# Kernel optimization log

Hardware: AMD Instinct MI355X
Metric: run time of the kernel (lower is better)

The kernel has to match this reference:

```python
import jax, jax.numpy as jnp
import numpy as np

B, NH, M, XD = 8192, 128, 4096, 1024
ALPHA_1, SIGMA_1 = 100.0, 0.02
MAX_ITER = 30  # FastBarrierProjectionNoUpper(max_iter=30)


def cayley(W):
    """Cayley orthogonalization of a (possibly rectangular) matrix (out, in)."""
    cout, cin = W.shape
    if cout < cin:
        return cayley(W.T).T
    U, V = W[:cin], W[cin:]                 # U: (cin,cin), V: (cout-cin,cin)
    I = jnp.eye(cin, dtype=W.dtype)
    A = U - U.T + V.T @ V                   # skew + Gram
    iIpA = jnp.linalg.inv(I + A)
    return jnp.concatenate([iIpA @ (I - A), -2.0 * V @ iIpA], axis=0)


def cayley_linear(x, W, b, alpha):
    Q = cayley(alpha * W / jnp.linalg.norm(W))
    return x @ Q.T + b


def project_no_upper(lower, f_tilde):
    """Projection of f_tilde onto {f : sum(f)=0, f >= lower} per row.
    f*(lam) = max(f_tilde - lam, lower); Newton on g(lam)=sum f*(lam)=0,
    iterated a fixed MAX_ITER times (matches the 30-iter barrier solver)."""
    lam0 = jnp.mean(f_tilde, axis=-1, keepdims=True)

    def step(lam, _):
        f = jnp.maximum(f_tilde - lam, lower)
        g = jnp.sum(f, axis=-1, keepdims=True)
        active = jnp.sum((f_tilde - lam > lower).astype(f.dtype), axis=-1, keepdims=True)
        dg = -jnp.maximum(active, 1.0)      # g'(lam), safeguarded
        return lam - g / dg, None

    lam, _ = jax.lax.scan(step, lam0, None, length=MAX_ITER)
    return jnp.maximum(f_tilde - lam, lower)


def setup_inputs() -> dict:
    key = jax.random.key(0)
    ks = jax.random.split(key, 8)
    h = jax.random.uniform(ks[0], (B, NH), dtype=jnp.float32)
    h = h / jnp.sum(h, axis=-1, keepdims=True)      # state lives on the simplex
    x = jax.random.normal(ks[1], (B, XD), dtype=jnp.float32)

    def mk_w(k, shape):
        return jax.random.normal(k, shape, dtype=jnp.float32) * 0.05

    W_hm = mk_w(ks[2], (M, NH))
    W_mm = mk_w(ks[3], (M, M))
    W_mh = mk_w(ks[4], (NH, M))
    W_ux = mk_w(ks[5], (M, XD))
    b_hm = jnp.zeros((M,), jnp.float32)
    b_mm = jnp.zeros((M,), jnp.float32)
    b_mh = jnp.zeros((NH,), jnp.float32)
    b_ux = jnp.zeros((M,), jnp.float32)
    # CayleyLinear alpha initialized to ||W||_F (so alpha*W/||W|| == W at init)
    a_hm = jnp.linalg.norm(W_hm)
    a_mm = jnp.linalg.norm(W_mm)
    a_mh = jnp.linalg.norm(W_mh)
    a_ux = jnp.linalg.norm(W_ux)
    return {"h": h, "x": x,
            "W_hm": W_hm, "b_hm": b_hm, "a_hm": a_hm,
            "W_mm": W_mm, "b_mm": b_mm, "a_mm": a_mm,
            "W_mh": W_mh, "b_mh": b_mh, "a_mh": a_mh,
            "W_ux": W_ux, "b_ux": b_ux, "a_ux": a_ux}


def reference(h, x, W_hm, b_hm, a_hm, W_mm, b_mm, a_mm,
              W_mh, b_mh, a_mh, W_ux, b_ux, a_ux):
    # _h_dot_raw (dropout identity in eval mode)
    z = cayley_linear(h, W_hm, b_hm, a_hm) + cayley_linear(x, W_ux, b_ux, a_ux)
    z = jax.nn.relu(z)
    z = jax.nn.relu(cayley_linear(z, W_mm, b_mm, a_mm))
    f_tilde = cayley_linear(z, W_mh, b_mh, a_mh)   # [B, NH]
    # barrier lower bound keeping h >= 0 forward-invariant
    lower = -ALPHA_1 * (jnp.exp(SIGMA_1 * h) - 1.0)
    return project_no_upper(lower, f_tilde)
```

## Files before the change

### kernel.cpp

```cpp
#include <hip/hip_runtime.h>
#include <math.h>

#define ALPHA_1 100.0f
#define SIGMA_1 0.02f

typedef unsigned short bf16_t;
typedef short  bf16x8  __attribute__((ext_vector_type(8)));
typedef float  floatx4 __attribute__((ext_vector_type(4)));

typedef __attribute__((address_space(1))) void glb_void;
typedef __attribute__((address_space(3))) void lds_void;

__device__ __forceinline__ float bf2f(bf16_t u){ return __uint_as_float(((unsigned)u)<<16); }
__device__ __forceinline__ bf16_t f2bf(float f){
  unsigned u = __float_as_uint(f);
  u += 0x7FFFu + ((u>>16)&1u);
  return (bf16_t)(u>>16);
}

__device__ __forceinline__ void split4(float4 v, ushort4& h, ushort4& l){
  h.x=f2bf(v.x); h.y=f2bf(v.y); h.z=f2bf(v.z); h.w=f2bf(v.w);
  l.x=f2bf(v.x-bf2f(h.x)); l.y=f2bf(v.y-bf2f(h.y));
  l.z=f2bf(v.z-bf2f(h.z)); l.w=f2bf(v.w-bf2f(h.w));
}

__device__ __forceinline__ float4 load4f(const float* p){ return *(const float4*)p; }
__device__ __forceinline__ float loadS(const float* p){ return *p; }
__device__ __forceinline__ float loadS(const bf16_t* p){ return bf2f(*p); }
__device__ __forceinline__ void storeS(float* p, float v){ *p = v; }
__device__ __forceinline__ void storeS(bf16_t* p, float v){ *p = f2bf(v); }

__device__ __forceinline__ void async_copy16(void* lds, const void* g){
  __builtin_amdgcn_global_load_lds((glb_void*)g, (lds_void*)lds, 16, 0, 0);
}

template<typename TC, int RELU>
__global__ __launch_bounds__(256) void mfma_nt_kernel(
    int Mm, int Nn, int Kk,
    const bf16_t* __restrict__ A, int lda,
    const bf16_t* __restrict__ B, int ldb,
    TC* __restrict__ C, int ldc,
    const float* __restrict__ bias)
{
  __shared__ bf16_t As[128*64];
  __shared__ bf16_t Bs[128*64];
  const int tid  = threadIdx.x;
  const int lane = tid & 63, wv = tid >> 6;
  const int m0 = (int)(blockIdx.y << 7), n0 = (int)(blockIdx.x << 7);
  const int wm = (wv >> 1) << 6, wn = (wv & 1) << 6;
  const int rbase = wv << 5;

  floatx4 acc[4][4] = {};

  for (int kk = 0; kk < Kk; kk += 64){
    __syncthreads();
#pragma unroll
    for (int q=0;q<4;q++){
      int row = rbase + (q<<3) + (lane>>3);
      int cg  = (lane&7) ^ (row&7);
      async_copy16(&As[(size_t)(rbase+(q<<3))<<6],
                   A + (size_t)(m0+row)*lda + kk + (cg<<3));
      async_copy16(&Bs[(size_t)(rbase+(q<<3))<<6],
                   B + (size_t)(n0+row)*ldb + kk + (cg<<3));
    }
    __syncthreads();
#pragma unroll
    for (int ks=0; ks<2; ks++){
      bf16x8 af[4], bf[4];
      int quad = lane>>4, mr = lane&15;
      int c = quad + (ks<<2);
#pragma unroll
      for (int i=0;i<4;i++){
        int rowa = wm + i*16 + mr;
        af[i] = *(const bf16x8*)&As[(rowa<<6) + ((c ^ (rowa&7))<<3)];
        int rowb = wn + i*16 + mr;
        bf[i] = *(const bf16x8*)&Bs[(rowb<<6) + ((c ^ (rowb&7))<<3)];
      }
#pragma unroll
      for (int i=0;i<4;i++)
#pragma unroll
        for (int j=0;j<4;j++)
          acc[i][j] = __builtin_amdgcn_mfma_f32_16x16x32_bf16(af[i], bf[j], acc[i][j], 0,0,0);
    }
  }
#pragma unroll
  for (int i=0;i<4;i++){
#pragma unroll
    for (int j=0;j<4;j++){
      int rbase2 = m0 + wm + i*16 + (lane>>4)*4;
      int col    = n0 + wn + j*16 + (lane&15);
      float bv = bias ? bias[col] : 0.0f;
#pragma unroll
      for (int r=0;r<4;r++){
        float v = acc[i][j][r] + bv;
        if (RELU) v = fmaxf(v, 0.0f);
        storeS(&C[(size_t)(rbase2+r)*ldc + col], v);
      }
    }
  }
}

template<typename TC>
__global__ __launch_bounds__(256) void fgemm_nt_kernel(
    int Mm, int Nn, int Kk,
    const float* __restrict__ A, int lda,
    const float* __restrict__ Bt, int ldb,
    TC* __restrict__ C, int ldc,
    float alpha, const float* __restrict__ alpha_ptr, float beta, int skipk)
{
  __shared__ bf16_t Ah[128*64], Al[128*64], Bh[128*64], Bl[128*64];
  const int tid = threadIdx.x;
  const int lane = tid & 63, wv = tid >> 6;
  int by = blockIdx.y; if (by >= skipk) by++;
  const int m0 = by << 7, n0 = blockIdx.x << 7;
  const int wm = (wv >> 1) << 6, wn = (wv & 1) << 6;
  floatx4 acc[4][4] = {};

  for (int kk = 0; kk < Kk; kk += 64){
    float4 va[8], vb[8];
#pragma unroll
    for (int i=0;i<8;i++){
      int idx = (tid<<3) + i;
      int row = idx >> 4;
      int cg  = idx & 15;
      va[i] = load4f(A  + (size_t)(m0+row)*lda + kk + (cg<<2));
      vb[i] = load4f(Bt + (size_t)(n0+row)*ldb + kk + (cg<<2));
    }
    __syncthreads();
#pragma unroll
    for (int i=0;i<8;i++){
      int idx = (tid<<3) + i;
      int row = idx >> 4, cg = idx & 15;
      int off = (row<<6) + (((cg>>1) ^ (row&7))<<3) + ((cg&1)<<2);
      ushort4 hv, lv; split4(va[i], hv, lv);
      *(ushort4*)&Ah[off] = hv; *(ushort4*)&Al[off] = lv;
      ushort4 hw, lw; split4(vb[i], hw, lw);
      *(ushort4*)&Bh[off] = hw; *(ushort4*)&Bl[off] = lw;
    }
    __syncthreads();
#pragma unroll
    for (int ks=0; ks<2; ks++){
      int quad = lane>>4, mr = lane&15;
      int c = quad + (ks<<2);
      bf16x8 ah[4], al[4], bh[4], bl[4];
#pragma unroll
      for (int i=0;i<4;i++){
        int rowa = wm + i*16 + mr; int sa = (rowa<<6) + ((c ^ (rowa&7))<<3);
        ah[i] = *(const bf16x8*)&Ah[sa]; al[i] = *(const bf16x8*)&Al[sa];
        int rowb = wn + i*16 + mr; int sb = (rowb<<6) + ((c ^ (rowb&7))<<3);
        bh[i] = *(const bf16x8*)&Bh[sb]; bl[i] = *(const bf16x8*)&Bl[sb];
      }
#pragma unroll
      for (int i=0;i<4;i++)
#pragma unroll
        for (int j=0;j<4;j++){
          acc[i][j] = __builtin_amdgcn_mfma_f32_16x16x32_bf16(ah[i], bl[j], acc[i][j], 0,0,0);
          acc[i][j] = __builtin_amdgcn_mfma_f32_16x16x32_bf16(al[i], bh[j], acc[i][j], 0,0,0);
          acc[i][j] = __builtin_amdgcn_mfma_f32_16x16x32_bf16(ah[i], bh[j], acc[i][j], 0,0,0);
        }
    }
    __syncthreads();
  }
  float am = alpha;
  if (alpha_ptr) am *= *alpha_ptr;
#pragma unroll
  for (int i=0;i<4;i++){
#pragma unroll
    for (int j=0;j<4;j++){
      int rb = m0 + wm + i*16 + (lane>>4)*4;
      int col = n0 + wn + j*16 + (lane&15);
#pragma unroll
      for (int r=0;r<4;r++){
        size_t off = (size_t)(rb+r)*ldc + col;
        float v = am * acc[i][j][r];
        if (beta != 0.0f) v = fmaf(beta, loadS(&C[off]), v);
        storeS(&C[off], v);
      }
    }
  }
}

__global__ __launch_bounds__(1024) void invert128_kernel(
    const float* __restrict__ src, int ld,
    float* __restrict__ dst, float* __restrict__ dstT)
{
  __shared__ float brow[2][8*36];
  const int t = threadIdx.x;
  const int r = t>>3, sub = t&7;
  const int lane = t & 63;
  const int cb = (sub&3)<<5;
  const bool isA = sub < 4;
  float own[32];
  if (isA){
#pragma unroll
    for (int i=0;i<32;i++) own[i] = src[(size_t)r*ld + cb + i];
  } else {
#pragma unroll
    for (int i=0;i<32;i++) own[i] = (cb+i == r) ? 1.0f : 0.0f;
  }
  for (int pb=0; pb<4; pb++){
#pragma unroll
    for (int pi=0; pi<32; pi++){
      const int p = (pb<<5) + pi;
      float f = __shfl(own[pi], (lane & 56) | pb);
      float* bw = brow[p & 1];
      if (r == p){
        float ip = 1.0f / f;
#pragma unroll
        for (int i=0;i<32;i++) own[i] *= ip;
#pragma unroll
        for (int i=0;i<8;i++){
          float4 v;
          v.x = own[(i<<2)+0]; v.y = own[(i<<2)+1];
          v.z = own[(i<<2)+2]; v.w = own[(i<<2)+3];
          *(float4*)&bw[sub*36 + (i<<2)] = v;
        }
      }
      __syncthreads();
      if (r != p){
#pragma unroll
        for (int i=0;i<8;i++){
          float4 b = *(const float4*)&bw[sub*36 + (i<<2)];
          own[(i<<2)+0] = fmaf(-f, b.x, own[(i<<2)+0]);
          own[(i<<2)+1] = fmaf(-f, b.y, own[(i<<2)+1]);
          own[(i<<2)+2] = fmaf(-f, b.z, own[(i<<2)+2]);
          own[(i<<2)+3] = fmaf(-f, b.w, own[(i<<2)+3]);
        }
      }
    }
  }
  if (!isA){
#pragma unroll
    for (int i=0;i<32;i++){
      dst [(size_t)r*128 + cb + i] = own[i];
      dstT[(size_t)(cb+i)*128 + r] = own[i];
    }
  }
}

__global__ __launch_bounds__(1024) void gj_prepL_kernel(
    const float* __restrict__ Mc, int n, int k,
    bf16_t* __restrict__ Gh, bf16_t* __restrict__ Gl,
    bf16_t* __restrict__ Th, bf16_t* __restrict__ Tl)
{
  __shared__ float brow[2][8*36];
  __shared__ float Pl[128*132];
  __shared__ float Ast[128*132];
  const int t = threadIdx.x;
  const int ib = blockIdx.x;
  const int r = t>>3, sub = t&7;
  const int lane = t & 63;
  const int cb = (sub&3)<<5;
  const bool isA = sub < 4;
  const float* D = Mc + ((size_t)(k<<7))*n + (k<<7);
  float own[32];
  if (isA){
#pragma unroll
    for (int q=0;q<32;q++) own[q] = D[(size_t)r*n + cb + q];
  } else {
#pragma unroll
    for (int q=0;q<32;q++) own[q] = (cb+q == r) ? 1.0f : 0.0f;
  }
  for (int pb=0; pb<4; pb++){
#pragma unroll
    for (int pi=0; pi<32; pi++){
      const int p = (pb<<5) + pi;
      float f = __shfl(own[pi], (lane & 56) | pb);
      float* bw = brow[p & 1];
      if (r == p){
        float ip = 1.0f / f;
#pragma unroll
        for (int q=0;q<32;q++) own[q] *= ip;
#pragma unroll
        for (int q=0;q<8;q++){
          float4 v;
          v.x=own[(q<<2)+0]; v.y=own[(q<<2)+1]; v.z=own[(q<<2)+2]; v.w=own[(q<<2)+3];
          *(float4*)&bw[sub*36 + (q<<2)] = v;
        }
      }
      __syncthreads();
      if (r != p){
#pragma unroll
        for (int q=0;q<8;q++){
          float4 b = *(const float4*)&bw[sub*36 + (q<<2)];
          own[(q<<2)+0] = fmaf(-f, b.x, own[(q<<2)+0]);
          own[(q<<2)+1] = fmaf(-f, b.y, own[(q<<2)+1]);
          own[(q<<2)+2] = fmaf(-f, b.z, own[(q<<2)+2]);
          own[(q<<2)+3] = fmaf(-f, b.w, own[(q<<2)+3]);
        }
      }
    }
  }
  if (!isA){
#pragma unroll
    for (int q=0;q<8;q++){
      float4 v;
      v.x=own[(q<<2)+0]; v.y=own[(q<<2)+1]; v.z=own[(q<<2)+2]; v.w=own[(q<<2)+3];
      *(float4*)&Pl[r*132 + cb + (q<<2)] = v;
      if (ib == k){
        ushort4 hv, lv; split4(v, hv, lv);
        *(ushort4*)&Gh[((size_t)k<<14) + (r<<7) + cb + (q<<2)] = hv;
        *(ushort4*)&Gl[((size_t)k<<14) + (r<<7) + cb + (q<<2)] = lv;
      }
    }
  }
  __syncthreads();
  if (ib == k) return;

  const float* Ski = Mc + ((size_t)(k<<7))*n + (ib<<7);
#pragma unroll
  for (int q=0;q<4;q++){
    int f4 = (t<<2) + q;
    int rr = f4>>5, c4 = (f4&31)<<2;
    *(float4*)&Ast[rr*132 + c4] = *(const float4*)&Ski[(size_t)rr*n + c4];
  }
  __syncthreads();
#pragma unroll
  for (int q=0;q<4;q++){
    int f4 = (t<<2) + q;
    int cc = f4>>5, r4 = (f4&31)<<2;
    float4 v;
    v.x = Ast[(r4+0)*132 + cc]; v.y = Ast[(r4+1)*132 + cc];
    v.z = Ast[(r4+2)*132 + cc]; v.w = Ast[(r4+3)*132 + cc];
    ushort4 hv, lv; split4(v, hv, lv);
    *(ushort4*)&Th[((size_t)ib<<14) + (cc<<7) + r4] = hv;
    *(ushort4*)&Tl[((size_t)ib<<14) + (cc<<7) + r4] = lv;
  }
  __syncthreads();

  const float* Sik = Mc + ((size_t)(ib<<7))*n + (k<<7);
#pragma unroll
  for (int q=0;q<4;q++){
    int f4 = (t<<2) + q;
    int rr = f4>>5, c4 = (f4&31)<<2;
    *(float4*)&Ast[rr*132 + c4] = *(const float4*)&Sik[(size_t)rr*n + c4];
  }
  __syncthreads();

  const int tx = t&31, ty = t>>5;
  const int r0 = ty<<2, c0 = tx<<2;
  float acc[4][4] = {};
  for (int kq=0; kq<128; kq++){
    float4 b = *(const float4*)&Pl[kq*132 + c0];
    float a0 = Ast[(r0+0)*132 + kq];
    float a1 = Ast[(r0+1)*132 + kq];
    float a2 = Ast[(r0+2)*132 + kq];
    float a3 = Ast[(r0+3)*132 + kq];
    acc[0][0]=fmaf(a0,b.x,acc[0][0]); acc[0][1]=fmaf(a0,b.y,acc[0][1]);
    acc[0][2]=fmaf(a0,b.z,acc[0][2]); acc[0][3]=fmaf(a0,b.w,acc[0][3]);
    acc[1][0]=fmaf(a1,b.x,acc[1][0]); acc[1][1]=fmaf(a1,b.y,acc[1][1]);
    acc[1][2]=fmaf(a1,b.z,acc[1][2]); acc[1][3]=fmaf(a1,b.w,acc[1][3]);
    acc[2][0]=fmaf(a2,b.x,acc[2][0]); acc[2][1]=fmaf(a2,b.y,acc[2][1]);
    acc[2][2]=fmaf(a2,b.z,acc[2][2]); acc[2][3]=fmaf(a2,b.w,acc[2][3]);
    acc[3][0]=fmaf(a3,b.x,acc[3][0]); acc[3][1]=fmaf(a3,b.y,acc[3][1]);
    acc[3][2]=fmaf(a3,b.z,acc[3][2]); acc[3][3]=fmaf(a3,b.w,acc[3][3]);
  }
#pragma unroll
  for (int rr=0;rr<4;rr++){
    float4 v; v.x=-acc[rr][0]; v.y=-acc[rr][1]; v.z=-acc[rr][2]; v.w=-acc[rr][3];
    ushort4 hv, lv; split4(v, hv, lv);
    *(ushort4*)&Gh[((size_t)ib<<14) + ((size_t)(r0+rr)<<7) + c0] = hv;
    *(ushort4*)&Gl[((size_t)ib<<14) + ((size_t)(r0+rr)<<7) + c0] = lv;
  }
}

__global__ __launch_bounds__(256) void gj_update_kernel(
    const float* __restrict__ Min, float* __restrict__ Mout, int n, int k,
    const bf16_t* __restrict__ Gh, const bf16_t* __restrict__ Gl,
    const bf16_t* __restrict__ Th, const bf16_t* __restrict__ Tl)
{
  const int bx = blockIdx.x, by = blockIdx.y;
  const int tid = threadIdx.x;
  if (bx == k){
    const bf16_t* sh = Gh + ((size_t)by<<14);
    const bf16_t* sl = Gl + ((size_t)by<<14);
    float* dst = Mout + ((size_t)(by<<7))*n + ((size_t)k<<7);
    for (int q=tid; q<4096; q+=256){
      int r=q>>5, c4=(q&31)<<2;
      ushort4 hv=*(const ushort4*)&sh[(r<<7)+c4];
      ushort4 lv=*(const ushort4*)&sl[(r<<7)+c4];
      float4 v; v.x=bf2f(hv.x)+bf2f(lv.x); v.y=bf2f(hv.y)+bf2f(lv.y);
                v.z=bf2f(hv.z)+bf2f(lv.z); v.w=bf2f(hv.w)+bf2f(lv.w);
      *(float4*)&dst[(size_t)r*n + c4] = v;
    }
    return;
  }
  __shared__ bf16_t Ah[128*64], Al[128*64], Bh[128*64], Bl[128*64];
  const int lane = tid & 63, wv = tid >> 6;
  const int wm = (wv >> 1) << 6, wn = (wv & 1) << 6;
  const bf16_t* gh = Gh + ((size_t)by<<14);
  const bf16_t* gl = Gl + ((size_t)by<<14);
  const bf16_t* th = Th + ((size_t)bx<<14);
  const bf16_t* tl = Tl + ((size_t)bx<<14);
  floatx4 acc[4][4] = {};

#pragma unroll
  for (int kk = 0; kk < 128; kk += 64){
    __syncthreads();
#pragma unroll
    for (int i=0;i<8;i++){
      int idx = (tid<<3) + i;
      int row = idx >> 4, cg = idx & 15;
      int off = (row<<6) + (((cg>>1) ^ (row&7))<<3) + ((cg&1)<<2);
      *(ushort4*)&Ah[off] = *(const ushort4*)&gh[(row<<7) + kk + (cg<<2)];
      *(ushort4*)&Al[off] = *(const ushort4*)&gl[(row<<7) + kk + (cg<<2)];
      *(ushort4*)&Bh[off] = *(const ushort4*)&th[(row<<7) + kk + (cg<<2)];
      *(ushort4*)&Bl[off] = *(const ushort4*)&tl[(row<<7) + kk + (cg<<2)];
    }
    __syncthreads();
#pragma unroll
    for (int ks=0; ks<2; ks++){
      int quad = lane>>4, mr = lane&15;
      int c = quad + (ks<<2);
      bf16x8 ah[4], al[4], bh[4], bl[4];
#pragma unroll
      for (int i=0;i<4;i++){
        int rowa = wm + i*16 + mr; int sa = (rowa<<6) + ((c ^ (rowa&7))<<3);
        ah[i] = *(const bf16x8*)&Ah[sa]; al[i] = *(const bf16x8*)&Al[sa];
        int rowb = wn + i*16 + mr; int sb = (rowb<<6) + ((c ^ (rowb&7))<<3);
        bh[i] = *(const bf16x8*)&Bh[sb]; bl[i] = *(const bf16x8*)&Bl[sb];
      }
#pragma unroll
      for (int i=0;i<4;i++)
#pragma unroll
        for (int j=0;j<4;j++){
          acc[i][j] = __builtin_amdgcn_mfma_f32_16x16x32_bf16(ah[i], bl[j], acc[i][j], 0,0,0);
          acc[i][j] = __builtin_amdgcn_mfma_f32_16x16x32_bf16(al[i], bh[j], acc[i][j], 0,0,0);
          acc[i][j] = __builtin_amdgcn_mfma_f32_16x16x32_bf16(ah[i], bh[j], acc[i][j], 0,0,0);
        }
    }
  }
  const int addin = (by != k);
#pragma unroll
  for (int i=0;i<4;i++)
#pragma unroll
    for (int j=0;j<4;j++){
      int rb = (by<<7) + wm + i*16 + ((lane>>4)<<2);
      int col = (bx<<7) + wn + j*16 + (lane&15);
#pragma unroll
      for (int r4=0;r4<4;r4++){
        size_t off = (size_t)(rb+r4)*n + col;
        float v = acc[i][j][r4];
        if (addin) v += Min[off];
        Mout[off] = v;
      }
    }
}

template<int TRANS>
__global__ __launch_bounds__(256) void gram_partial_kernel(
    const float* __restrict__ V, int ldv, int n, int Ks,
    float* __restrict__ Gp)
{
  __shared__ float Vi[16][132];
  __shared__ float Vj[16][132];
  const int cj = blockIdx.x, ci = blockIdx.y, z = blockIdx.z;
  const int tid = threadIdx.x;
  const int i0 = ci<<7, j0 = cj<<7;
  const int tx = tid&15, ty = tid>>4;
  float acc[8][8] = {};
  for (int k0 = z*Ks; k0 < (z+1)*Ks; k0 += 16){
    if (TRANS == 0){
      for (int q=tid; q<512; q+=256){
        int kr = q>>5, c4 = (q&31)<<2;
        *(float4*)&Vi[kr][c4] = *(const float4*)&V[(size_t)(k0+kr)*ldv + i0 + c4];
        *(float4*)&Vj[kr][c4] = *(const float4*)&V[(size_t)(k0+kr)*ldv + j0 + c4];
      }
    } else {
      for (int q=tid; q<512; q+=256){
        int c = q>>2, qq = (q&3)<<2;
        float4 a = *(const float4*)&V[(size_t)(i0+c)*ldv + k0 + qq];
        Vi[qq+0][c]=a.x; Vi[qq+1][c]=a.y; Vi[qq+2][c]=a.z; Vi[qq+3][c]=a.w;
        float4 b = *(const float4*)&V[(size_t)(j0+c)*ldv + k0 + qq];
        Vj[qq+0][c]=b.x; Vj[qq+1][c]=b.y; Vj[qq+2][c]=b.z; Vj[qq+3][c]=b.w;
      }
    }
    __syncthreads();
#pragma unroll
    for (int kr=0; kr<16; kr++){
      float a[8], b[8];
      *(float4*)&a[0] = *(const float4*)&Vi[kr][(ty<<3)];
      *(float4*)&a[4] = *(const float4*)&Vi[kr][(ty<<3)+4];
      *(float4*)&b[0] = *(const float4*)&Vj[kr][(tx<<3)];
      *(float4*)&b[4] = *(const float4*)&Vj[kr][(tx<<3)+4];
#pragma unroll
      for (int i=0;i<8;i++)
#pragma unroll
        for (int jj=0;jj<8;jj++) acc[i][jj] = fmaf(a[i], b[jj], acc[i][jj]);
    }
    __syncthreads();
  }
#pragma unroll
  for (int i=0;i<8;i++)
#pragma unroll
    for (int jj=0;jj<8;jj++)
      Gp[(size_t)z*n*n + (size_t)(i0+(ty<<3)+i)*n + j0+(tx<<3)+jj] = acc[i][jj];
}

__global__ void sumsq_kernel(const float* __restrict__ w, int n, float* __restrict__ acc){
  float s = 0.0f;
  for (int i = blockIdx.x*blockDim.x + threadIdx.x; i < n; i += gridDim.x*blockDim.x){
    float v = w[i]; s = fmaf(v, v, s);
  }
#pragma unroll
  for (int o=32;o;o>>=1) s += __shfl_xor(s, o);
  if ((threadIdx.x & 63) == 0) atomicAdd(acc, s);
}

__global__ void scales_kernel(float* scal, const float* a0, const float* a1,
                              const float* a2, const float* a3){
  if (threadIdx.x==0 && blockIdx.x==0){
    float s;
    s = a0[0]/sqrtf(scal[0]); scal[4]=s; scal[8]=s*s;
    s = a1[0]/sqrtf(scal[1]); scal[5]=s; scal[9]=s*s;
    s = a2[0]/sqrtf(scal[2]); scal[6]=s; scal[10]=s*s;
    s = a3[0]/sqrtf(scal[3]); scal[7]=s; scal[11]=s*s;
  }
}

__global__ void build_mm_kernel(const float* __restrict__ W, const float* __restrict__ scal,
                                float* __restrict__ Mo){
  int j = (blockIdx.x<<4) + (threadIdx.x&15);
  int i = (blockIdx.y<<4) + (threadIdx.x>>4);
  float s = scal[5];
  float a = s*(W[((size_t)i<<12)+j] - W[((size_t)j<<12)+i]);
  Mo[((size_t)i<<12)+j] = ((i==j)?1.0f:0.0f) + a;
}

__global__ void build_rect_kernel(const float* __restrict__ W, int ldw, int transw, int n,
      const float* __restrict__ Gp, int S,
      const float* __restrict__ scal, int sidx, int sidx2,
      float* __restrict__ Mo){
  int j = (blockIdx.x<<4)+(threadIdx.x&15);
  int i = (blockIdx.y<<4)+(threadIdx.x>>4);
  float s = scal[sidx], s2 = scal[sidx2];
  float wij = transw ? W[(size_t)j*ldw+i] : W[(size_t)i*ldw+j];
  float wji = transw ? W[(size_t)i*ldw+j] : W[(size_t)j*ldw+i];
  float g = 0.0f;
  for (int ss=0; ss<S; ss++) g += Gp[(size_t)ss*n*n + (size_t)i*n + j];
  Mo[(size_t)i*n + j] = ((i==j)?1.0f:0.0f) + s*(wij - wji) + s2*g;
}

template<typename TD>
__global__ void qtop_kernel(const float* __restrict__ X, int n,
                            TD* __restrict__ dst, int ldd){
  int j = blockIdx.x*blockDim.x + threadIdx.x;
  int i = blockIdx.y;
  if (j<n) storeS(&dst[(size_t)i*ldd+j],
                  2.0f*X[(size_t)i*n+j] - ((i==j)?1.0f:0.0f));
}

__global__ void transposeF_kernel(const float* __restrict__ src, int ls,
                                  float* __restrict__ dst, int ld){
  __shared__ float t[32][33];
  int c0 = blockIdx.x<<5, r0 = blockIdx.y<<5;
  int tx = threadIdx.x & 31, ty = threadIdx.x >> 5;
#pragma unroll
  for (int i=0;i<4;i++) t[ty+i*8][tx] = src[(size_t)(r0+ty+i*8)*ls + c0+tx];
  __syncthreads();
#pragma unroll
  for (int i=0;i<4;i++) dst[(size_t)(c0+ty+i*8)*ld + r0+tx] = t[tx][ty+i*8];
}

__global__ void pack_A_kernel(const float* __restrict__ h, const float* __restrict__ x,
                              bf16_t* __restrict__ Ap){
  int c = blockIdx.x*blockDim.x + threadIdx.x;
  int m = blockIdx.y;
  if (c >= 2176) return;
  float v;
  if (c < 128)       v = h[(size_t)m*128 + c];
  else if (c < 1152) v = x[(size_t)m*1024 + (c-128)];
  else {
    float xv = x[(size_t)m*1024 + (c-1152)];
    v = xv - bf2f(f2bf(xv));
  }
  Ap[(size_t)m*2176 + c] = f2bf(v);
}

__global__ void dup_kernel(bf16_t* __restrict__ Bp){
  int c = blockIdx.x*blockDim.x + threadIdx.x;
  int r = blockIdx.y;
  Bp[(size_t)r*2176 + 1152 + c] = Bp[(size_t)r*2176 + 128 + c];
}

__global__ void addvec_kernel(const float* __restrict__ a, const float* __restrict__ b,
                              float* __restrict__ c, int n){
  int i = blockIdx.x*blockDim.x + threadIdx.x;
  if (i<n) c[i] = a[i] + b[i];
}

__global__ __launch_bounds__(256) void project_kernel(
    const float* __restrict__ ft, const float* __restrict__ h, float* __restrict__ out){
  int row  = (blockIdx.x<<2) + (threadIdx.x>>6);
  int lane = threadIdx.x & 63;
  const float* fr = ft + ((size_t)row<<7);
  const float* hr = h  + ((size_t)row<<7);
  float f0 = fr[lane], f1 = fr[lane+64];
  float l0 = -ALPHA_1*(expf(SIGMA_1*hr[lane])   - 1.0f);
  float l1 = -ALPHA_1*(expf(SIGMA_1*hr[lane+64])- 1.0f);
  float s = f0 + f1;
#pragma unroll
  for (int o=32;o;o>>=1) s += __shfl_xor(s, o);
  float lam = s * (1.0f/128.0f);
  for (int it=0; it<30; it++){
    float a0 = f0 - lam, a1 = f1 - lam;
    float g = fmaxf(a0,l0) + fmaxf(a1,l1);
    float c = (a0>l0 ? 1.0f:0.0f) + (a1>l1 ? 1.0f:0.0f);
#pragma unroll
    for (int o=32;o;o>>=1){ g += __shfl_xor(g,o); c += __shfl_xor(c,o); }
    lam += g / fmaxf(c, 1.0f);
  }
  out[((size_t)row<<7)+lane]    = fmaxf(f0-lam, l0);
  out[((size_t)row<<7)+lane+64] = fmaxf(f1-lam, l1);
}

template<typename TC, int RELU>
static inline void mfma_nt(hipStream_t st, int Mm, int Nn, int Kk,
    const bf16_t* A, int lda, const bf16_t* B, int ldb, TC* C, int ldc,
    const float* bias){
  dim3 grid(Nn>>7, Mm>>7);
  mfma_nt_kernel<TC,RELU><<<grid, 256, 0, st>>>(Mm,Nn,Kk,A,lda,B,ldb,C,ldc,bias);
}

template<typename TC>
static inline void fgemm(hipStream_t st, int Mm, int Nn, int Kk,
    const float* A, int lda, const float* Bt, int ldb, TC* C, int ldc,
    float alpha, const float* aptr, float beta){
  dim3 grid(Nn>>7, Mm>>7);
  fgemm_nt_kernel<TC><<<grid, 256, 0, st>>>(Mm,Nn,Kk,A,lda,Bt,ldb,C,ldc,
                                            alpha,aptr,beta, 1<<30);
}

static void gj_inverse2(hipStream_t st, float* M, float* Mtmp, int n,
                        bf16_t* Gh, bf16_t* Gl, bf16_t* Th, bf16_t* Tl){
  int nb = n >> 7;
  float* cur = M; float* nxt = Mtmp;
  for (int k=0;k<nb;k++){
    gj_prepL_kernel<<<nb, 1024, 0, st>>>(cur, n, k, Gh, Gl, Th, Tl);
    dim3 grid(nb, nb);
    gj_update_kernel<<<grid, 256, 0, st>>>(cur, nxt, n, k, Gh, Gl, Th, Tl);
    float* t = cur; cur = nxt; nxt = t;
  }
}

extern "C" void kernel_launch(void* const* d_in, const int* in_sizes, int n_in,
                              void* d_out, int out_size, void* d_ws, size_t ws_size,
                              hipStream_t stream){
  (void)in_sizes; (void)n_in; (void)out_size; (void)ws_size;
  const float* h    = (const float*)d_in[0];
  const float* x    = (const float*)d_in[1];
  const float* Whm  = (const float*)d_in[2];
  const float* bhm  = (const float*)d_in[3];
  const float* ahm  = (const float*)d_in[4];
  const float* Wmm  = (const float*)d_in[5];
  const float* bmm  = (const float*)d_in[6];
  const float* amm  = (const float*)d_in[7];
  const float* Wmh  = (const float*)d_in[8];
  const float* bmh  = (const float*)d_in[9];
  const float* amh  = (const float*)d_in[10];
  const float* Wux  = (const float*)d_in[11];
  const float* bux  = (const float*)d_in[12];
  const float* auxs = (const float*)d_in[13];
  float* out = (float*)d_out;

  char* wp = (char*)d_ws;
  auto alloc = [&](size_t bytes)->void*{
    void* p = (void*)wp; wp += (bytes + 255) & ~(size_t)255; return p; };
  float*  scal   = (float*)alloc(4096);
  float*  Mhm    = (float*)alloc((size_t)128*128*4);
  float*  Mmh    = (float*)alloc((size_t)128*128*4);
  float*  P128   = (float*)alloc((size_t)128*128*4);
  float*  PT128  = (float*)alloc((size_t)128*128*4);
  bf16_t* GhB    = (bf16_t*)alloc((size_t)32*16384*2);
  bf16_t* GlB    = (bf16_t*)alloc((size_t)32*16384*2);
  bf16_t* ThB    = (bf16_t*)alloc((size_t)32*16384*2);
  bf16_t* TlB    = (bf16_t*)alloc((size_t)32*16384*2);
  bf16_t* Qmh_b  = (bf16_t*)alloc((size_t)128*4096*2);
  float*  bsum   = (float*)alloc((size_t)4096*4);
  bf16_t* Bp     = (bf16_t*)alloc((size_t)4096*2176*2);
  float*  R1     = (float*)alloc((size_t)4096*4096*4);
  float*  R2     = (float*)alloc((size_t)4096*4096*4);
  bf16_t* Qmmb   = (bf16_t*)alloc((size_t)4096*4096*2);
  float*  gram23 = R1;
  float*  WmhTv  = R1 + (size_t)1024*1024;
  float*  Mmm  = R1;
  bf16_t* Ap   = (bf16_t*)R1;
  bf16_t* z2   = (bf16_t*)R1;
  float*  Mux  = R2 + (size_t)1024*1024;
  float*  XuxT = R2 + (size_t)5*1024*1024;
  float*  Gp1  = R2 + (size_t)6*1024*1024;
  bf16_t* z    = (bf16_t*)R2;
  float*  ftl  = R2;

  hipMemsetAsync(scal, 0, 16*sizeof(float), stream);
  sumsq_kernel<<<512,256,0,stream>>>(Whm, 4096*128,  scal+0);
  sumsq_kernel<<<512,256,0,stream>>>(Wmm, 4096*4096, scal+1);
  sumsq_kernel<<<512,256,0,stream>>>(Wmh, 128*4096,  scal+2);
  sumsq_kernel<<<512,256,0,stream>>>(Wux, 4096*1024, scal+3);
  scales_kernel<<<1,1,0,stream>>>(scal, ahm, amm, amh, auxs);

  gram_partial_kernel<0><<<dim3(8,8,4),256,0,stream>>>(
      Wux + (size_t)1024*1024, 1024, 1024, 768, Gp1);
  build_rect_kernel<<<dim3(64,64),256,0,stream>>>(Wux,1024,0,1024, Gp1,4, scal,7,11, Mux);
  gj_inverse2(stream, Mux, R1, 1024, GhB, GlB, ThB, TlB);
  transposeF_kernel<<<dim3(32,32),256,0,stream>>>(Mux, 1024, XuxT, 1024);
  qtop_kernel<bf16_t><<<dim3(4,1024),256,0,stream>>>(Mux, 1024, Bp+128, 2176);
  fgemm<bf16_t>(stream, 3072,1024,1024, Wux+(size_t)1024*1024,1024, XuxT,1024,
                Bp+(size_t)1024*2176+128, 2176, -2.0f,&scal[7], 0.0f);

  gram_partial_kernel<0><<<dim3(1,1,31),256,0,stream>>>(
      Whm + (size_t)128*128, 128, 128, 128, gram23);
  build_rect_kernel<<<dim3(8,8),256,0,stream>>>(Whm,128,0,128, gram23,31, scal,4,8, Mhm);
  invert128_kernel<<<1,1024,0,stream>>>(Mhm,128,P128,PT128);
  qtop_kernel<bf16_t><<<dim3(1,128),256,0,stream>>>(P128, 128, Bp, 2176);
  fgemm<bf16_t>(stream, 3968,128,128, Whm+128*128,128, PT128,128,
                Bp+(size_t)128*2176, 2176, -2.0f,&scal[4], 0.0f);

  gram_partial_kernel<1><<<dim3(1,1,31),256,0,stream>>>(
      Wmh + 128, 4096, 128, 128, gram23);
  build_rect_kernel<<<dim3(8,8),256,0,stream>>>(Wmh,4096,1,128, gram23,31, scal,6,10, Mmh);
  invert128_kernel<<<1,1024,0,stream>>>(Mmh,128,P128,PT128);
  qtop_kernel<bf16_t><<<dim3(1,128),256,0,stream>>>(PT128, 128, Qmh_b, 4096);
  transposeF_kernel<<<dim3(124,4),256,0,stream>>>(Wmh+128, 4096, WmhTv, 128);
  fgemm<bf16_t>(stream, 128,3968,128, PT128,128, WmhTv,128,
                Qmh_b+128, 4096, -2.0f,&scal[6], 0.0f);

  build_mm_kernel<<<dim3(256,256),256,0,stream>>>(Wmm, scal, Mmm);
  gj_inverse2(stream, Mmm, R2, 4096, GhB, GlB, ThB, TlB);
  qtop_kernel<bf16_t><<<dim3(16,4096),256,0,stream>>>(Mmm, 4096, Qmmb, 4096);

  pack_A_kernel<<<dim3(9,8192),256,0,stream>>>(h, x, Ap);
  dup_kernel<<<dim3(4,4096),256,0,stream>>>(Bp);
  addvec_kernel<<<16,256,0,stream>>>(bhm, bux, bsum, 4096);

  mfma_nt<bf16_t,1>(stream, 8192,4096,2176, Ap,2176, Bp,2176, z,4096, bsum);
  mfma_nt<bf16_t,1>(stream, 8192,4096,4096, z,4096, Qmmb,4096, z2,4096, bmm);
  mfma_nt<float,0>(stream, 8192, 128,4096, z2,4096, Qmh_b,4096, ftl,128, bmh);

  project_kernel<<<2048,256,0,stream>>>(ftl, h, out);
}
```

Measured before the change: 6.347 ms.

## Pipeline block Gauss-Jordan: fuse next-panel prep with trailing update

Restructures the blocked Gauss-Jordan inverse so that each step first updates the next pivot block-column and row (stepA). A second kernel then runs the next panel's prep concurrently with the rest of the trailing update (stepB), using double-buffered G/T panel buffers. This removes the serial single-row-of-blocks prep launch between update launches, where only nb blocks kept the GPU busy. Update tiles now use 1024-thread blocks with a 2x2 MFMA tile per wave instead of 256 threads with 4x4. That changes occupancy and register use, and the heavy prep blocks may become stragglers inside stepB.

Result: faster. 5.696 ms (-10.3%).

```diff
diff --git a/kernel.cpp b/kernel.cpp
--- a/kernel.cpp
+++ b/kernel.cpp
@@ -238,16 +238,16 @@
   }
 }
 
-__global__ __launch_bounds__(1024) void gj_prepL_kernel(
-    const float* __restrict__ Mc, int n, int k,
+
+__device__ void prep1024(
+    const float* __restrict__ Mc, int n, int k, int ib,
     bf16_t* __restrict__ Gh, bf16_t* __restrict__ Gl,
-    bf16_t* __restrict__ Th, bf16_t* __restrict__ Tl)
-{
-  __shared__ float brow[2][8*36];
-  __shared__ float Pl[128*132];
-  __shared__ float Ast[128*132];
-  const int t = threadIdx.x;
-  const int ib = blockIdx.x;
+    bf16_t* __restrict__ Th, bf16_t* __restrict__ Tl,
+    char* smraw, int t)
+{
+  float* browB = (float*)smraw;
+  float* Pl    = (float*)(smraw + 2304);
+  float* Ast   = (float*)(smraw + 69888);
   const int r = t>>3, sub = t&7;
   const int lane = t & 63;
   const int cb = (sub&3)<<5;
@@ -266,7 +266,7 @@
     for (int pi=0; pi<32; pi++){
       const int p = (pb<<5) + pi;
       float f = __shfl(own[pi], (lane & 56) | pb);
-      float* bw = brow[p & 1];
+      float* bw = browB + (p & 1)*288;
       if (r == p){
         float ip = 1.0f / f;
 #pragma unroll
@@ -364,18 +364,18 @@
   }
 }
 
-__global__ __launch_bounds__(256) void gj_update_kernel(
+__device__ void update_tile1024(
     const float* __restrict__ Min, float* __restrict__ Mout, int n, int k,
+    int by, int bx,
     const bf16_t* __restrict__ Gh, const bf16_t* __restrict__ Gl,
-    const bf16_t* __restrict__ Th, const bf16_t* __restrict__ Tl)
-{
-  const int bx = blockIdx.x, by = blockIdx.y;
-  const int tid = threadIdx.x;
+    const bf16_t* __restrict__ Th, const bf16_t* __restrict__ Tl,
+    char* sm, int tid)
+{
   if (bx == k){
     const bf16_t* sh = Gh + ((size_t)by<<14);
     const bf16_t* sl = Gl + ((size_t)by<<14);
     float* dst = Mout + ((size_t)(by<<7))*n + ((size_t)k<<7);
-    for (int q=tid; q<4096; q+=256){
+    for (int q=tid; q<4096; q+=1024){
       int r=q>>5, c4=(q&31)<<2;
       ushort4 hv=*(const ushort4*)&sh[(r<<7)+c4];
       ushort4 lv=*(const ushort4*)&sl[(r<<7)+c4];
@@ -385,21 +385,22 @@
     }
     return;
   }
-  __shared__ bf16_t Ah[128*64], Al[128*64], Bh[128*64], Bl[128*64];
+  bf16_t* Ah=(bf16_t*)sm;           bf16_t* Al=(bf16_t*)(sm+16384);
+  bf16_t* Bh=(bf16_t*)(sm+32768);   bf16_t* Bl=(bf16_t*)(sm+49152);
   const int lane = tid & 63, wv = tid >> 6;
-  const int wm = (wv >> 1) << 6, wn = (wv & 1) << 6;
+  const int wm = (wv >> 2) << 5, wn = (wv & 3) << 5;
   const bf16_t* gh = Gh + ((size_t)by<<14);
   const bf16_t* gl = Gl + ((size_t)by<<14);
   const bf16_t* th = Th + ((size_t)bx<<14);
   const bf16_t* tl = Tl + ((size_t)bx<<14);
-  floatx4 acc[4][4] = {};
+  floatx4 acc[2][2] = {};
 
 #pragma unroll
   for (int kk = 0; kk < 128; kk += 64){
     __syncthreads();
 #pragma unroll
-    for (int i=0;i<8;i++){
-      int idx = (tid<<3) + i;
+    for (int s=0;s<2;s++){
+      int idx = tid + (s<<10);
       int row = idx >> 4, cg = idx & 15;
       int off = (row<<6) + (((cg>>1) ^ (row&7))<<3) + ((cg&1)<<2);
       *(ushort4*)&Ah[off] = *(const ushort4*)&gh[(row<<7) + kk + (cg<<2)];
@@ -412,18 +413,18 @@
     for (int ks=0; ks<2; ks++){
       int quad = lane>>4, mr = lane&15;
       int c = quad + (ks<<2);
-      bf16x8 ah[4], al[4], bh[4], bl[4];
-#pragma unroll
-      for (int i=0;i<4;i++){
+      bf16x8 ah[2], al[2], bh[2], bl[2];
+#pragma unroll
+      for (int i=0;i<2;i++){
         int rowa = wm + i*16 + mr; int sa = (rowa<<6) + ((c ^ (rowa&7))<<3);
         ah[i] = *(const bf16x8*)&Ah[sa]; al[i] = *(const bf16x8*)&Al[sa];
         int rowb = wn + i*16 + mr; int sb = (rowb<<6) + ((c ^ (rowb&7))<<3);
         bh[i] = *(const bf16x8*)&Bh[sb]; bl[i] = *(const bf16x8*)&Bl[sb];
       }
 #pragma unroll
-      for (int i=0;i<4;i++)
-#pragma unroll
-        for (int j=0;j<4;j++){
+      for (int i=0;i<2;i++)
+#pragma unroll
+        for (int j=0;j<2;j++){
           acc[i][j] = __builtin_amdgcn_mfma_f32_16x16x32_bf16(ah[i], bl[j], acc[i][j], 0,0,0);
           acc[i][j] = __builtin_amdgcn_mfma_f32_16x16x32_bf16(al[i], bh[j], acc[i][j], 0,0,0);
           acc[i][j] = __builtin_amdgcn_mfma_f32_16x16x32_bf16(ah[i], bh[j], acc[i][j], 0,0,0);
@@ -432,9 +433,9 @@
   }
   const int addin = (by != k);
 #pragma unroll
-  for (int i=0;i<4;i++)
-#pragma unroll
-    for (int j=0;j<4;j++){
+  for (int i=0;i<2;i++)
+#pragma unroll
+    for (int j=0;j<2;j++){
       int rb = (by<<7) + wm + i*16 + ((lane>>4)<<2);
       int col = (bx<<7) + wn + j*16 + (lane&15);
 #pragma unroll
@@ -445,6 +446,59 @@
         Mout[off] = v;
       }
     }
+}
+
+__global__ __launch_bounds__(1024) void gj_prep0_kernel(
+    const float* __restrict__ M, int n,
+    bf16_t* Gh, bf16_t* Gl, bf16_t* Th, bf16_t* Tl)
+{
+  __shared__ char sm[137472] __attribute__((aligned(16)));
+  prep1024(M, n, 0, blockIdx.x, Gh, Gl, Th, Tl, sm, threadIdx.x);
+}
+
+__global__ __launch_bounds__(1024) void gj_stepA_kernel(
+    const float* __restrict__ Min, float* __restrict__ Mout, int n, int k,
+    const bf16_t* __restrict__ Gh, const bf16_t* __restrict__ Gl,
+    const bf16_t* __restrict__ Th, const bf16_t* __restrict__ Tl)
+{
+  __shared__ char sm[65536] __attribute__((aligned(16)));
+  const int nb = n >> 7;
+  const int bid = blockIdx.x;
+  int by, bx;
+  if (bid < nb){ by = bid; bx = k+1; }
+  else { by = k+1; bx = bid-nb; if (bx >= k+1) bx++; }
+  update_tile1024(Min, Mout, n, k, by, bx, Gh, Gl, Th, Tl, sm, threadIdx.x);
+}
+
+__global__ __launch_bounds__(1024) void gj_stepB_kernel(
+    const float* __restrict__ Min, float* __restrict__ Mout, int n, int k,
+    const bf16_t* __restrict__ Gh, const bf16_t* __restrict__ Gl,
+    const bf16_t* __restrict__ Th, const bf16_t* __restrict__ Tl,
+    bf16_t* Gnh, bf16_t* Gnl, bf16_t* Tnh, bf16_t* Tnl)
+{
+  __shared__ char sm[137472] __attribute__((aligned(16)));
+  const int nb = n >> 7;
+  const int bid = blockIdx.x, tid = threadIdx.x;
+  if (bid < nb){
+    prep1024(Mout, n, k+1, bid, Gnh, Gnl, Tnh, Tnl, sm, tid);
+  } else {
+    int q = bid - nb;
+    int by = q/(nb-1), bx = q - by*(nb-1);
+    if (by >= k+1) by++;
+    if (bx >= k+1) bx++;
+    update_tile1024(Min, Mout, n, k, by, bx, Gh, Gl, Th, Tl, sm, tid);
+  }
+}
+
+__global__ __launch_bounds__(1024) void gj_stepL_kernel(
+    const float* __restrict__ Min, float* __restrict__ Mout, int n, int k,
+    const bf16_t* __restrict__ Gh, const bf16_t* __restrict__ Gl,
+    const bf16_t* __restrict__ Th, const bf16_t* __restrict__ Tl)
+{
+  __shared__ char sm[65536] __attribute__((aligned(16)));
+  const int nb = n >> 7;
+  int by = blockIdx.x / nb, bx = blockIdx.x - by*nb;
+  update_tile1024(Min, Mout, n, k, by, bx, Gh, Gl, Th, Tl, sm, threadIdx.x);
 }
 
 template<int TRANS>
@@ -631,15 +685,25 @@
                                             alpha,aptr,beta, 1<<30);
 }
 
-static void gj_inverse2(hipStream_t st, float* M, float* Mtmp, int n,
-                        bf16_t* Gh, bf16_t* Gl, bf16_t* Th, bf16_t* Tl){
-  int nb = n >> 7;
-  float* cur = M; float* nxt = Mtmp;
-  for (int k=0;k<nb;k++){
-    gj_prepL_kernel<<<nb, 1024, 0, st>>>(cur, n, k, Gh, Gl, Th, Tl);
-    dim3 grid(nb, nb);
-    gj_update_kernel<<<grid, 256, 0, st>>>(cur, nxt, n, k, Gh, Gl, Th, Tl);
-    float* t = cur; cur = nxt; nxt = t;
+static void gj_inverse4(hipStream_t st, float* M, float* Mtmp, int n,
+    bf16_t* Gh, bf16_t* Gl, bf16_t* Th, bf16_t* Tl){
+  const int nb = n >> 7;
+  const size_t gstep = (size_t)nb << 14;
+  gj_prep0_kernel<<<nb, 1024, 0, st>>>(M, n, Gh, Gl, Th, Tl);
+  for (int k=0; k<nb; k++){
+    const float* Min = (k&1) ? Mtmp : M;
+    float* Mout      = (k&1) ? M : Mtmp;
+    const size_t pc = (size_t)(k&1)*gstep, pn = (size_t)((k&1)^1)*gstep;
+    if (k < nb-1){
+      gj_stepA_kernel<<<2*nb-1, 1024, 0, st>>>(Min, Mout, n, k,
+          Gh+pc, Gl+pc, Th+pc, Tl+pc);
+      gj_stepB_kernel<<<nb + (nb-1)*(nb-1), 1024, 0, st>>>(Min, Mout, n, k,
+          Gh+pc, Gl+pc, Th+pc, Tl+pc,
+          Gh+pn, Gl+pn, Th+pn, Tl+pn);
+    } else {
+      gj_stepL_kernel<<<nb*nb, 1024, 0, st>>>(Min, Mout, n, k,
+          Gh+pc, Gl+pc, Th+pc, Tl+pc);
+    }
   }
 }
 
@@ -671,10 +735,10 @@
   float*  Mmh    = (float*)alloc((size_t)128*128*4);
   float*  P128   = (float*)alloc((size_t)128*128*4);
   float*  PT128  = (float*)alloc((size_t)128*128*4);
-  bf16_t* GhB    = (bf16_t*)alloc((size_t)32*16384*2);
-  bf16_t* GlB    = (bf16_t*)alloc((size_t)32*16384*2);
-  bf16_t* ThB    = (bf16_t*)alloc((size_t)32*16384*2);
-  bf16_t* TlB    = (bf16_t*)alloc((size_t)32*16384*2);
+  bf16_t* GhB    = (bf16_t*)alloc((size_t)2*32*16384*2);
+  bf16_t* GlB    = (bf16_t*)alloc((size_t)2*32*16384*2);
+  bf16_t* ThB    = (bf16_t*)alloc((size_t)2*32*16384*2);
+  bf16_t* TlB    = (bf16_t*)alloc((size_t)2*32*16384*2);
   bf16_t* Qmh_b  = (bf16_t*)alloc((size_t)128*4096*2);
   float*  bsum   = (float*)alloc((size_t)4096*4);
   bf16_t* Bp     = (bf16_t*)alloc((size_t)4096*2176*2);
@@ -702,7 +766,7 @@
   gram_partial_kernel<0><<<dim3(8,8,4),256,0,stream>>>(
       Wux + (size_t)1024*1024, 1024, 1024, 768, Gp1);
   build_rect_kernel<<<dim3(64,64),256,0,stream>>>(Wux,1024,0,1024, Gp1,4, scal,7,11, Mux);
-  gj_inverse2(stream, Mux, R1, 1024, GhB, GlB, ThB, TlB);
+  gj_inverse4(stream, Mux, R1, 1024, GhB, GlB, ThB, TlB);
   transposeF_kernel<<<dim3(32,32),256,0,stream>>>(Mux, 1024, XuxT, 1024);
   qtop_kernel<bf16_t><<<dim3(4,1024),256,0,stream>>>(Mux, 1024, Bp+128, 2176);
   fgemm<bf16_t>(stream, 3072,1024,1024, Wux+(size_t)1024*1024,1024, XuxT,1024,
@@ -726,7 +790,7 @@
                 Qmh_b+128, 4096, -2.0f,&scal[6], 0.0f);
 
   build_mm_kernel<<<dim3(256,256),256,0,stream>>>(Wmm, scal, Mmm);
-  gj_inverse2(stream, Mmm, R2, 4096, GhB, GlB, ThB, TlB);
+  gj_inverse4(stream, Mmm, R2, 4096, GhB, GlB, ThB, TlB);
   qtop_kernel<bf16_t><<<dim3(16,4096),256,0,stream>>>(Mmm, 4096, Qmmb, 4096);
 
   pack_A_kernel<<<dim3(9,8192),256,0,stream>>>(h, x, Ap);
```
